# Kernel optimization log

Hardware: AMD Instinct MI355X
Metric: run time of the kernel (lower is better)

Reference implementation:

```python
import jax, jax.numpy as jnp
import numpy as np

N, D, P, R, T, K = 200000, 128, 4096, 4, 3, 16

def setup_inputs() -> dict:
    key = jax.random.key(0)
    ks = jax.random.split(key, 9)
    return {
        "node_embeds": jax.random.normal(ks[0], (N, D), jnp.float32),
        "node_pairs": jax.random.randint(ks[1], (P, 2), 0, N),
        "node_type_ids": jax.random.randint(ks[2], (N,), 0, T),
        "neighbor_idx": jax.random.randint(ks[3], (P, 2, R, K), 0, N),
        "delta_t": jax.random.uniform(ks[4], (P, 2, R, K), jnp.float32),
        "W_phi": jax.random.normal(ks[5], (T, D, D), jnp.float32) * 0.05,
        "W_zeta": jax.random.normal(ks[6], (2 * D,), jnp.float32) * 0.05,
        "W_beta_w": jax.random.normal(ks[7], (R, D, D), jnp.float32) * 0.05,
        "W_beta_b": jax.random.normal(ks[8], (R, D), jnp.float32) * 0.05,
    }

def reference(node_embeds, node_pairs, node_type_ids, neighbor_idx, delta_t,
              W_phi, W_zeta, W_beta_w, W_beta_b):
    n = node_embeds.shape[0]
    # per-node type-specific linear: compute all types then select (T small)
    H_all = jnp.einsum('nd,tde->tne', node_embeds, W_phi)        # [T,N,D]
    H = H_all[node_type_ids, jnp.arange(n)]                      # [N,D]
    # micro attention: e = W_zeta([h_n; h_s]) * exp(-dt), softmax over K neighbors
    zn, zs = W_zeta[:D], W_zeta[D:]
    h_n = H[neighbor_idx]                                        # [P,2,R,K,D]
    e_n = jnp.einsum('psrkd,d->psrk', h_n, zn)
    e_s = jnp.einsum('psd,d->ps', H[node_pairs], zs)             # [P,2]
    e = (e_n + e_s[:, :, None, None]) * jnp.exp(-delta_t)        # [P,2,R,K]
    alpha = jax.nn.softmax(e, axis=-1)
    # meso: attention-weighted aggregation per relation, then per-relation linear
    h_nei = node_embeds[neighbor_idx]                            # [P,2,R,K,D]
    h_agg = jnp.einsum('psrk,psrkd->psrd', alpha, h_nei)         # [P,2,R,D]
    h_beta = jnp.einsum('psrd,rde->psre', h_agg, W_beta_w) + W_beta_b
    # macro: average over both pair sides and relations, sigmoid combine
    x_tilde = h_beta.mean(axis=(1, 2))                           # [P,D]
    return jax.nn.sigmoid(x_tilde)
```

## Files before the change

### kernel.cpp

```cpp
#include <hip/hip_runtime.h>
#include <hip/hip_bf16.h>

#define NN 200000
#define D 128
#define P 4096
#define R 4
#define T 3
#define K 16

__device__ __forceinline__ float bf2f(unsigned int u) {
    union { unsigned int i; float f; } c;
    c.i = u << 16;
    return c.f;
}
__device__ __forceinline__ unsigned short f2bf(float x) {
    union { float f; unsigned int i; } c; c.f = x;
    unsigned int r = c.i + 0x7FFFu + ((c.i >> 16) & 1u);
    return (unsigned short)(r >> 16);
}
__device__ __forceinline__ float ldE(const void* p, size_t i, int f32) {
    return f32 ? ((const float*)p)[i] : bf2f(((const unsigned short*)p)[i]);
}
__device__ __forceinline__ void ld8(const void* p, size_t off, int f32, float* o) {
    if (f32) {
        const float* q = (const float*)p + off;
        float4 a = *(const float4*)q;
        float4 b = *(const float4*)(q + 4);
        o[0]=a.x; o[1]=a.y; o[2]=a.z; o[3]=a.w;
        o[4]=b.x; o[5]=b.y; o[6]=b.z; o[7]=b.w;
    } else {
        uint4 r = *(const uint4*)((const unsigned short*)p + off);
        o[0]=bf2f(r.x & 0xffffu); o[1]=bf2f(r.x >> 16);
        o[2]=bf2f(r.y & 0xffffu); o[3]=bf2f(r.y >> 16);
        o[4]=bf2f(r.z & 0xffffu); o[5]=bf2f(r.z >> 16);
        o[6]=bf2f(r.w & 0xffffu); o[7]=bf2f(r.w >> 16);
    }
}

__global__ void prep_kernel(const unsigned short* __restrict__ emb_u,
                            const void* __restrict__ W_phi,
                            const void* __restrict__ W_zeta,
                            int* __restrict__ gflag,
                            float* __restrict__ ws_v, float* __restrict__ ws_u) {
    __shared__ int sbad[2];
    const int tid = threadIdx.x;
    const int t   = blockIdx.x;
    int bad = 0;
    #pragma unroll
    for (int i = 0; i < 4; ++i) {
        unsigned short u = emb_u[(size_t)(blockIdx.x * 512 + tid * 4 + i) * 2 * 97];
        unsigned int e = (u >> 7) & 0xFFu;
        if (e >= 147u) bad = 1;
    }
    int anyb = __any(bad) ? 1 : 0;
    if ((tid & 63) == 0) sbad[tid >> 6] = anyb;
    __syncthreads();
    const int f32 = sbad[0] | sbad[1];
    if (t == 0 && tid == 0) *gflag = f32;

    const int d = tid;
    const size_t rb = (size_t)(t * D + d) * D;
    float av = 0.f, au = 0.f;
    for (int e = 0; e < D; e += 8) {
        float w[8], zn[8], zs[8];
        ld8(W_phi, rb + e, f32, w);
        ld8(W_zeta, e, f32, zn);
        ld8(W_zeta, D + e, f32, zs);
        #pragma unroll
        for (int q = 0; q < 8; ++q) { av += w[q] * zn[q]; au += w[q] * zs[q]; }
    }
    ws_v[t * D + d] = av;
    ws_u[t * D + d] = au;
}

__global__ __launch_bounds__(256, 4) void fused_all(
    const void* __restrict__ emb,
    const int* __restrict__ pairs,
    const int* __restrict__ types,
    const int* __restrict__ nbr,
    const void* __restrict__ dlt,
    const void* __restrict__ W_bw,
    const void* __restrict__ W_bb,
    const float* __restrict__ ws_v,
    const float* __restrict__ ws_u,
    const int* __restrict__ flag,
    void* __restrict__ out)
{
    __shared__ __align__(16) float vsh[T * D];
    __shared__ __align__(16) float ush[T * D];
    __shared__ __align__(16) float gsh[2][2][R][D];
    __shared__ __align__(16) float ysh[2][2][D];

    const int f32  = *flag;
    const int tid  = threadIdx.x;
    const int wv   = tid >> 6;
    const int l    = tid & 63;
    const int pr   = wv >> 1;
    const int s    = wv & 1;
    const int p    = blockIdx.x * 2 + pr;
    const int rsub = l >> 4;
    const int ch   = l & 15;
    const int base = p * 2 * R * K + s * 64;

    for (int i = tid; i < T * D; i += 256) { vsh[i] = ws_v[i]; ush[i] = ws_u[i]; }
    __syncthreads();

    const int nb  = nbr[base + l];
    const float dtv = ldE(dlt, (size_t)base + l, f32);
    const int tp  = types[nb];

    float es;
    {
        int ns = pairs[p * 2 + s];
        int ts = types[ns];
        float a = ldE(emb, (size_t)ns * D + 2 * l,     f32) * ush[ts * D + 2 * l]
                + ldE(emb, (size_t)ns * D + 2 * l + 1, f32) * ush[ts * D + 2 * l + 1];
        #pragma unroll
        for (int off = 1; off <= 32; off <<= 1) a += __shfl_xor(a, off, 64);
        es = a;
    }

    const unsigned short* eu = (const unsigned short*)emb;

    if (!f32) {
        int snb[4];
        uint4 cur[4], nxt[4];
        #pragma unroll
        for (int i = 0; i < 4; ++i) snb[i] = __shfl(nb, i * 4 + rsub, 64);
        #pragma unroll
        for (int i = 0; i < 4; ++i)
            cur[i] = *(const uint4*)(eu + (size_t)snb[i] * D + ch * 8);

        #pragma unroll
        for (int r = 0; r < R; ++r) {
            float sdt[4]; int stp[4];
            #pragma unroll
            for (int i = 0; i < 4; ++i) {
                int srcl = r * 16 + i * 4 + rsub;
                sdt[i] = __shfl(dtv, srcl, 64);
                stp[i] = __shfl(tp,  srcl, 64);
            }
            if (r < 3) {
                #pragma unroll
                for (int i = 0; i < 4; ++i) snb[i] = __shfl(nb, (r + 1) * 16 + i * 4 + rsub, 64);
                #pragma unroll
                for (int i = 0; i < 4; ++i)
                    nxt[i] = *(const uint4*)(eu + (size_t)snb[i] * D + ch * 8);
            }
            float ef[4];
            #pragma unroll
            for (int i = 0; i < 4; ++i) {
                const float* vp = vsh + stp[i] * D + ch * 8;
                float4 v0 = *(const float4*)vp;
                float4 v1 = *(const float4*)(vp + 4);
                float a = 0.f;
                a += bf2f(cur[i].x & 0xffffu) * v0.x + bf2f(cur[i].x >> 16) * v0.y;
                a += bf2f(cur[i].y & 0xffffu) * v0.z + bf2f(cur[i].y >> 16) * v0.w;
                a += bf2f(cur[i].z & 0xffffu) * v1.x + bf2f(cur[i].z >> 16) * v1.y;
                a += bf2f(cur[i].w & 0xffffu) * v1.z + bf2f(cur[i].w >> 16) * v1.w;
                #pragma unroll
                for (int off = 1; off <= 8; off <<= 1) a += __shfl_xor(a, off, 64);
                ef[i] = (a + es) * __expf(-sdt[i]);
            }
            float m = fmaxf(fmaxf(ef[0], ef[1]), fmaxf(ef[2], ef[3]));
            m = fmaxf(m, __shfl_xor(m, 16, 64));
            m = fmaxf(m, __shfl_xor(m, 32, 64));
            float al[4], ssum = 0.f;
            #pragma unroll
            for (int i = 0; i < 4; ++i) { al[i] = __expf(ef[i] - m); ssum += al[i]; }
            ssum += __shfl_xor(ssum, 16, 64);
            ssum += __shfl_xor(ssum, 32, 64);
            float inv = 1.f / ssum;
            float acc[8] = {0.f,0.f,0.f,0.f,0.f,0.f,0.f,0.f};
            #pragma unroll
            for (int i = 0; i < 4; ++i) {
                float a = al[i] * inv;
                acc[0] += a * bf2f(cur[i].x & 0xffffu); acc[1] += a * bf2f(cur[i].x >> 16);
                acc[2] += a * bf2f(cur[i].y & 0xffffu); acc[3] += a * bf2f(cur[i].y >> 16);
                acc[4] += a * bf2f(cur[i].z & 0xffffu); acc[5] += a * bf2f(cur[i].z >> 16);
                acc[6] += a * bf2f(cur[i].w & 0xffffu); acc[7] += a * bf2f(cur[i].w >> 16);
            }
            #pragma unroll
            for (int q = 0; q < 8; ++q) {
                acc[q] += __shfl_xor(acc[q], 16, 64);
                acc[q] += __shfl_xor(acc[q], 32, 64);
            }
            if (rsub == 0) {
                *(float4*)(&gsh[pr][s][r][ch * 8])     = make_float4(acc[0], acc[1], acc[2], acc[3]);
                *(float4*)(&gsh[pr][s][r][ch * 8 + 4]) = make_float4(acc[4], acc[5], acc[6], acc[7]);
            }
            #pragma unroll
            for (int i = 0; i < 4; ++i) cur[i] = nxt[i];
        }
    } else {
        #pragma unroll
        for (int r = 0; r < R; ++r) {
            int snb[4]; float sdt[4]; int stp[4];
            #pragma unroll
            for (int i = 0; i < 4; ++i) {
                int srcl = r * 16 + i * 4 + rsub;
                snb[i] = __shfl(nb,  srcl, 64);
                sdt[i] = __shfl(dtv, srcl, 64);
                stp[i] = __shfl(tp,  srcl, 64);
            }
            float rv[4][8];
            #pragma unroll
            for (int i = 0; i < 4; ++i) ld8(emb, (size_t)snb[i] * D + ch * 8, 1, rv[i]);
            float ef[4];
            #pragma unroll
            for (int i = 0; i < 4; ++i) {
                const float* vp = vsh + stp[i] * D + ch * 8;
                float a = 0.f;
                #pragma unroll
                for (int q = 0; q < 8; ++q) a += rv[i][q] * vp[q];
                #pragma unroll
                for (int off = 1; off <= 8; off <<= 1) a += __shfl_xor(a, off, 64);
                ef[i] = (a + es) * __expf(-sdt[i]);
            }
            float m = fmaxf(fmaxf(ef[0], ef[1]), fmaxf(ef[2], ef[3]));
            m = fmaxf(m, __shfl_xor(m, 16, 64));
            m = fmaxf(m, __shfl_xor(m, 32, 64));
            float al[4], ssum = 0.f;
            #pragma unroll
            for (int i = 0; i < 4; ++i) { al[i] = __expf(ef[i] - m); ssum += al[i]; }
            ssum += __shfl_xor(ssum, 16, 64);
            ssum += __shfl_xor(ssum, 32, 64);
            float inv = 1.f / ssum;
            float acc[8] = {0.f,0.f,0.f,0.f,0.f,0.f,0.f,0.f};
            #pragma unroll
            for (int i = 0; i < 4; ++i) {
                float a = al[i] * inv;
                #pragma unroll
                for (int q = 0; q < 8; ++q) acc[q] += a * rv[i][q];
            }
            #pragma unroll
            for (int q = 0; q < 8; ++q) {
                acc[q] += __shfl_xor(acc[q], 16, 64);
                acc[q] += __shfl_xor(acc[q], 32, 64);
            }
            if (rsub == 0) {
                *(float4*)(&gsh[pr][s][r][ch * 8])     = make_float4(acc[0], acc[1], acc[2], acc[3]);
                *(float4*)(&gsh[pr][s][r][ch * 8 + 4]) = make_float4(acc[4], acc[5], acc[6], acc[7]);
            }
        }
    }
    __syncthreads();

    float y[8] = {0.f,0.f,0.f,0.f,0.f,0.f,0.f,0.f};
    const unsigned short* Wu = (const unsigned short*)W_bw;
    #pragma unroll
    for (int rr = 0; rr < 2; ++rr) {
        const int r = s * 2 + rr;
        #pragma unroll 8
        for (int dd = 0; dd < 32; ++dd) {
            const int d = rsub * 32 + dd;
            float gd = gsh[pr][0][r][d] + gsh[pr][1][r][d];
            size_t wo = ((size_t)(r * D + d)) * D + ch * 8;
            if (!f32) {
                uint4 wr = *(const uint4*)(Wu + wo);
                y[0] += gd * bf2f(wr.x & 0xffffu); y[1] += gd * bf2f(wr.x >> 16);
                y[2] += gd * bf2f(wr.y & 0xffffu); y[3] += gd * bf2f(wr.y >> 16);
                y[4] += gd * bf2f(wr.z & 0xffffu); y[5] += gd * bf2f(wr.z >> 16);
                y[6] += gd * bf2f(wr.w & 0xffffu); y[7] += gd * bf2f(wr.w >> 16);
            } else {
                float wb[8]; ld8(W_bw, wo, 1, wb);
                #pragma unroll
                for (int q = 0; q < 8; ++q) y[q] += gd * wb[q];
            }
        }
    }
    #pragma unroll
    for (int q = 0; q < 8; ++q) {
        y[q] += __shfl_xor(y[q], 16, 64);
        y[q] += __shfl_xor(y[q], 32, 64);
    }
    if (rsub == 0) {
        *(float4*)(&ysh[pr][s][ch * 8])     = make_float4(y[0], y[1], y[2], y[3]);
        *(float4*)(&ysh[pr][s][ch * 8 + 4]) = make_float4(y[4], y[5], y[6], y[7]);
    }
    __syncthreads();

    if (s == 0 && rsub == 0) {
        float bs[8] = {0.f,0.f,0.f,0.f,0.f,0.f,0.f,0.f};
        #pragma unroll
        for (int r = 0; r < R; ++r) {
            float bb[8]; ld8(W_bb, (size_t)r * D + ch * 8, f32, bb);
            #pragma unroll
            for (int q = 0; q < 8; ++q) bs[q] += bb[q];
        }
        float o[8];
        #pragma unroll
        for (int q = 0; q < 8; ++q) {
            int e = ch * 8 + q;
            float x = (ysh[pr][0][e] + ysh[pr][1][e] + 2.f * bs[q]) * 0.125f;
            o[q] = 1.f / (1.f + __expf(-x));
        }
        size_t ob = (size_t)p * D + ch * 8;
        if (f32) {
            *(float4*)((float*)out + ob)     = make_float4(o[0], o[1], o[2], o[3]);
            *(float4*)((float*)out + ob + 4) = make_float4(o[4], o[5], o[6], o[7]);
        } else {
            uint4 pk;
            pk.x = (unsigned int)f2bf(o[0]) | ((unsigned int)f2bf(o[1]) << 16);
            pk.y = (unsigned int)f2bf(o[2]) | ((unsigned int)f2bf(o[3]) << 16);
            pk.z = (unsigned int)f2bf(o[4]) | ((unsigned int)f2bf(o[5]) << 16);
            pk.w = (unsigned int)f2bf(o[6]) | ((unsigned int)f2bf(o[7]) << 16);
            *(uint4*)((unsigned short*)out + ob) = pk;
        }
    }
}

extern "C" void kernel_launch(void* const* d_in, const int* in_sizes, int n_in,
                              void* d_out, int out_size, void* d_ws, size_t ws_size,
                              hipStream_t stream) {
    const void* emb    = d_in[0];
    const int*  pairs  = (const int*)d_in[1];
    const int*  types  = (const int*)d_in[2];
    const int*  nbr    = (const int*)d_in[3];
    const void* dlt    = d_in[4];
    const void* W_phi  = d_in[5];
    const void* W_zeta = d_in[6];
    const void* W_bw   = d_in[7];
    const void* W_bb   = d_in[8];

    int*   flag = (int*)d_ws;
    float* ws_v = (float*)d_ws + 64;
    float* ws_u = ws_v + T * D;

    prep_kernel<<<dim3(T), dim3(128), 0, stream>>>((const unsigned short*)emb,
                                                   W_phi, W_zeta, flag, ws_v, ws_u);
    fused_all<<<dim3(P / 2), dim3(256), 0, stream>>>(emb, pairs, types, nbr, dlt,
                                                     W_bw, W_bb, ws_v, ws_u, flag, d_out);
}
```

Before: 244.9 us.

## Assign one wave per (side, relation) with one pair per 512-thread block

Restructures the fused kernel so each 512-thread block handles one pair and each of its 8 waves processes one (side, relation) slice, replacing the per-wave serial loop over four relations. All neighbor gathers are issued up front, before the shared-memory staging barrier, so memory latency overlaps the setup. The W_beta projection is redistributed across all waves with a staggered row order and a reduction through shared memory. The change raises memory parallelism and occupancy, at the cost of more blocks, extra barriers and more weight re-reads per pair.

```diff
diff --git a/kernel.cpp b/kernel.cpp
--- a/kernel.cpp
+++ b/kernel.cpp
@@ -73,7 +73,7 @@
     ws_u[t * D + d] = au;
 }
 
-__global__ __launch_bounds__(256, 4) void fused_all(
+__global__ __launch_bounds__(512, 8) void fused_all(
     const void* __restrict__ emb,
     const int* __restrict__ pairs,
     const int* __restrict__ types,
@@ -88,31 +88,49 @@
 {
     __shared__ __align__(16) float vsh[T * D];
     __shared__ __align__(16) float ush[T * D];
-    __shared__ __align__(16) float gsh[2][2][R][D];
-    __shared__ __align__(16) float ysh[2][2][D];
+    __shared__ __align__(16) float gsh[2][R][D];
+    __shared__ __align__(16) float gsum[R][D];
+    __shared__ __align__(16) float ysh[R][D];
 
     const int f32  = *flag;
     const int tid  = threadIdx.x;
     const int wv   = tid >> 6;
     const int l    = tid & 63;
-    const int pr   = wv >> 1;
-    const int s    = wv & 1;
-    const int p    = blockIdx.x * 2 + pr;
+    const int s    = wv >> 2;
+    const int r    = wv & 3;
+    const int p    = blockIdx.x;
     const int rsub = l >> 4;
     const int ch   = l & 15;
-    const int base = p * 2 * R * K + s * 64;
-
-    for (int i = tid; i < T * D; i += 256) { vsh[i] = ws_v[i]; ush[i] = ws_u[i]; }
-    __syncthreads();
-
-    const int nb  = nbr[base + l];
-    const float dtv = ldE(dlt, (size_t)base + l, f32);
-    const int tp  = types[nb];
+    const int base = p * 2 * R * K + s * R * K + r * K;
+
+    const int k   = l & 15;
+    const int nb  = nbr[base + k];
+    const float dtv = ldE(dlt, (size_t)(base + k), f32);
+    const int ns  = pairs[p * 2 + s];
+
+    int snb[4];
+    #pragma unroll
+    for (int i = 0; i < 4; ++i) snb[i] = __shfl(nb, i * 4 + rsub, 64);
+
+    const unsigned short* eu = (const unsigned short*)emb;
+    uint4 cur[4];
+    float rv[4][8];
+    if (!f32) {
+        #pragma unroll
+        for (int i = 0; i < 4; ++i)
+            cur[i] = *(const uint4*)(eu + (size_t)snb[i] * D + ch * 8);
+    } else {
+        #pragma unroll
+        for (int i = 0; i < 4; ++i) ld8(emb, (size_t)snb[i] * D + ch * 8, 1, rv[i]);
+    }
+    const int tp = types[nb];
+    const int ts = types[ns];
+
+    for (int i = tid; i < T * D; i += 512) { vsh[i] = ws_v[i]; ush[i] = ws_u[i]; }
+    __syncthreads();
 
     float es;
     {
-        int ns = pairs[p * 2 + s];
-        int ts = types[ns];
         float a = ldE(emb, (size_t)ns * D + 2 * l,     f32) * ush[ts * D + 2 * l]
                 + ldE(emb, (size_t)ns * D + 2 * l + 1, f32) * ush[ts * D + 2 * l + 1];
         #pragma unroll
@@ -120,182 +138,137 @@
         es = a;
     }
 
-    const unsigned short* eu = (const unsigned short*)emb;
-
+    float sdt[4]; int stp[4];
+    #pragma unroll
+    for (int i = 0; i < 4; ++i) {
+        sdt[i] = __shfl(dtv, i * 4 + rsub, 64);
+        stp[i] = __shfl(tp,  i * 4 + rsub, 64);
+    }
+
+    float ef[4];
     if (!f32) {
-        int snb[4];
-        uint4 cur[4], nxt[4];
-        #pragma unroll
-        for (int i = 0; i < 4; ++i) snb[i] = __shfl(nb, i * 4 + rsub, 64);
-        #pragma unroll
-        for (int i = 0; i < 4; ++i)
-            cur[i] = *(const uint4*)(eu + (size_t)snb[i] * D + ch * 8);
-
-        #pragma unroll
-        for (int r = 0; r < R; ++r) {
-            float sdt[4]; int stp[4];
-            #pragma unroll
-            for (int i = 0; i < 4; ++i) {
-                int srcl = r * 16 + i * 4 + rsub;
-                sdt[i] = __shfl(dtv, srcl, 64);
-                stp[i] = __shfl(tp,  srcl, 64);
-            }
-            if (r < 3) {
-                #pragma unroll
-                for (int i = 0; i < 4; ++i) snb[i] = __shfl(nb, (r + 1) * 16 + i * 4 + rsub, 64);
-                #pragma unroll
-                for (int i = 0; i < 4; ++i)
-                    nxt[i] = *(const uint4*)(eu + (size_t)snb[i] * D + ch * 8);
-            }
-            float ef[4];
-            #pragma unroll
-            for (int i = 0; i < 4; ++i) {
-                const float* vp = vsh + stp[i] * D + ch * 8;
-                float4 v0 = *(const float4*)vp;
-                float4 v1 = *(const float4*)(vp + 4);
-                float a = 0.f;
-                a += bf2f(cur[i].x & 0xffffu) * v0.x + bf2f(cur[i].x >> 16) * v0.y;
-                a += bf2f(cur[i].y & 0xffffu) * v0.z + bf2f(cur[i].y >> 16) * v0.w;
-                a += bf2f(cur[i].z & 0xffffu) * v1.x + bf2f(cur[i].z >> 16) * v1.y;
-                a += bf2f(cur[i].w & 0xffffu) * v1.z + bf2f(cur[i].w >> 16) * v1.w;
-                #pragma unroll
-                for (int off = 1; off <= 8; off <<= 1) a += __shfl_xor(a, off, 64);
-                ef[i] = (a + es) * __expf(-sdt[i]);
-            }
-            float m = fmaxf(fmaxf(ef[0], ef[1]), fmaxf(ef[2], ef[3]));
-            m = fmaxf(m, __shfl_xor(m, 16, 64));
-            m = fmaxf(m, __shfl_xor(m, 32, 64));
-            float al[4], ssum = 0.f;
-            #pragma unroll
-            for (int i = 0; i < 4; ++i) { al[i] = __expf(ef[i] - m); ssum += al[i]; }
-            ssum += __shfl_xor(ssum, 16, 64);
-            ssum += __shfl_xor(ssum, 32, 64);
-            float inv = 1.f / ssum;
-            float acc[8] = {0.f,0.f,0.f,0.f,0.f,0.f,0.f,0.f};
-            #pragma unroll
-            for (int i = 0; i < 4; ++i) {
-                float a = al[i] * inv;
-                acc[0] += a * bf2f(cur[i].x & 0xffffu); acc[1] += a * bf2f(cur[i].x >> 16);
-                acc[2] += a * bf2f(cur[i].y & 0xffffu); acc[3] += a * bf2f(cur[i].y >> 16);
-                acc[4] += a * bf2f(cur[i].z & 0xffffu); acc[5] += a * bf2f(cur[i].z >> 16);
-                acc[6] += a * bf2f(cur[i].w & 0xffffu); acc[7] += a * bf2f(cur[i].w >> 16);
-            }
-            #pragma unroll
-            for (int q = 0; q < 8; ++q) {
-                acc[q] += __shfl_xor(acc[q], 16, 64);
-                acc[q] += __shfl_xor(acc[q], 32, 64);
-            }
-            if (rsub == 0) {
-                *(float4*)(&gsh[pr][s][r][ch * 8])     = make_float4(acc[0], acc[1], acc[2], acc[3]);
-                *(float4*)(&gsh[pr][s][r][ch * 8 + 4]) = make_float4(acc[4], acc[5], acc[6], acc[7]);
-            }
-            #pragma unroll
-            for (int i = 0; i < 4; ++i) cur[i] = nxt[i];
+        #pragma unroll
+        for (int i = 0; i < 4; ++i) {
+            const float* vp = vsh + stp[i] * D + ch * 8;
+            float4 v0 = *(const float4*)vp;
+            float4 v1 = *(const float4*)(vp + 4);
+            float a = 0.f;
+            a += bf2f(cur[i].x & 0xffffu) * v0.x + bf2f(cur[i].x >> 16) * v0.y;
+            a += bf2f(cur[i].y & 0xffffu) * v0.z + bf2f(cur[i].y >> 16) * v0.w;
+            a += bf2f(cur[i].z & 0xffffu) * v1.x + bf2f(cur[i].z >> 16) * v1.y;
+            a += bf2f(cur[i].w & 0xffffu) * v1.z + bf2f(cur[i].w >> 16) * v1.w;
+            #pragma unroll
+            for (int off = 1; off <= 8; off <<= 1) a += __shfl_xor(a, off, 64);
+            ef[i] = (a + es) * __expf(-sdt[i]);
         }
     } else {
         #pragma unroll
-        for (int r = 0; r < R; ++r) {
-            int snb[4]; float sdt[4]; int stp[4];
-            #pragma unroll
-            for (int i = 0; i < 4; ++i) {
-                int srcl = r * 16 + i * 4 + rsub;
-                snb[i] = __shfl(nb,  srcl, 64);
-                sdt[i] = __shfl(dtv, srcl, 64);
-                stp[i] = __shfl(tp,  srcl, 64);
-            }
-            float rv[4][8];
-            #pragma unroll
-            for (int i = 0; i < 4; ++i) ld8(emb, (size_t)snb[i] * D + ch * 8, 1, rv[i]);
-            float ef[4];
-            #pragma unroll
-            for (int i = 0; i < 4; ++i) {
-                const float* vp = vsh + stp[i] * D + ch * 8;
-                float a = 0.f;
-                #pragma unroll
-                for (int q = 0; q < 8; ++q) a += rv[i][q] * vp[q];
-                #pragma unroll
-                for (int off = 1; off <= 8; off <<= 1) a += __shfl_xor(a, off, 64);
-                ef[i] = (a + es) * __expf(-sdt[i]);
-            }
-            float m = fmaxf(fmaxf(ef[0], ef[1]), fmaxf(ef[2], ef[3]));
-            m = fmaxf(m, __shfl_xor(m, 16, 64));
-            m = fmaxf(m, __shfl_xor(m, 32, 64));
-            float al[4], ssum = 0.f;
-            #pragma unroll
-            for (int i = 0; i < 4; ++i) { al[i] = __expf(ef[i] - m); ssum += al[i]; }
-            ssum += __shfl_xor(ssum, 16, 64);
-            ssum += __shfl_xor(ssum, 32, 64);
-            float inv = 1.f / ssum;
-            float acc[8] = {0.f,0.f,0.f,0.f,0.f,0.f,0.f,0.f};
-            #pragma unroll
-            for (int i = 0; i < 4; ++i) {
-                float a = al[i] * inv;
-                #pragma unroll
-                for (int q = 0; q < 8; ++q) acc[q] += a * rv[i][q];
-            }
-            #pragma unroll
-            for (int q = 0; q < 8; ++q) {
-                acc[q] += __shfl_xor(acc[q], 16, 64);
-                acc[q] += __shfl_xor(acc[q], 32, 64);
-            }
-            if (rsub == 0) {
-                *(float4*)(&gsh[pr][s][r][ch * 8])     = make_float4(acc[0], acc[1], acc[2], acc[3]);
-                *(float4*)(&gsh[pr][s][r][ch * 8 + 4]) = make_float4(acc[4], acc[5], acc[6], acc[7]);
-            }
-        }
+        for (int i = 0; i < 4; ++i) {
+            const float* vp = vsh + stp[i] * D + ch * 8;
+            float a = 0.f;
+            #pragma unroll
+            for (int q = 0; q < 8; ++q) a += rv[i][q] * vp[q];
+            #pragma unroll
+            for (int off = 1; off <= 8; off <<= 1) a += __shfl_xor(a, off, 64);
+            ef[i] = (a + es) * __expf(-sdt[i]);
+        }
+    }
+
+    float m = fmaxf(fmaxf(ef[0], ef[1]), fmaxf(ef[2], ef[3]));
+    m = fmaxf(m, __shfl_xor(m, 16, 64));
+    m = fmaxf(m, __shfl_xor(m, 32, 64));
+    float al[4], ssum = 0.f;
+    #pragma unroll
+    for (int i = 0; i < 4; ++i) { al[i] = __expf(ef[i] - m); ssum += al[i]; }
+    ssum += __shfl_xor(ssum, 16, 64);
+    ssum += __shfl_xor(ssum, 32, 64);
+    float inv = 1.f / ssum;
+
+    float acc[8] = {0.f,0.f,0.f,0.f,0.f,0.f,0.f,0.f};
+    if (!f32) {
+        #pragma unroll
+        for (int i = 0; i < 4; ++i) {
+            float a = al[i] * inv;
+            acc[0] += a * bf2f(cur[i].x & 0xffffu); acc[1] += a * bf2f(cur[i].x >> 16);
+            acc[2] += a * bf2f(cur[i].y & 0xffffu); acc[3] += a * bf2f(cur[i].y >> 16);
+            acc[4] += a * bf2f(cur[i].z & 0xffffu); acc[5] += a * bf2f(cur[i].z >> 16);
+            acc[6] += a * bf2f(cur[i].w & 0xffffu); acc[7] += a * bf2f(cur[i].w >> 16);
+        }
+    } else {
+        #pragma unroll
+        for (int i = 0; i < 4; ++i) {
+            float a = al[i] * inv;
+            #pragma unroll
+            for (int q = 0; q < 8; ++q) acc[q] += a * rv[i][q];
+        }
+    }
+    #pragma unroll
+    for (int q = 0; q < 8; ++q) {
+        acc[q] += __shfl_xor(acc[q], 16, 64);
+        acc[q] += __shfl_xor(acc[q], 32, 64);
+    }
+    if (rsub == 0) {
+        *(float4*)(&gsh[s][r][ch * 8])     = make_float4(acc[0], acc[1], acc[2], acc[3]);
+        *(float4*)(&gsh[s][r][ch * 8 + 4]) = make_float4(acc[4], acc[5], acc[6], acc[7]);
+    }
+    __syncthreads();
+
+    {
+        const int r2 = tid >> 7, d2 = tid & 127;
+        gsum[r2][d2] = gsh[0][r2][d2] + gsh[1][r2][d2];
     }
     __syncthreads();
 
     float y[8] = {0.f,0.f,0.f,0.f,0.f,0.f,0.f,0.f};
+    const int ch8  = l & 7;
+    const int dgrp = l >> 3;
     const unsigned short* Wu = (const unsigned short*)W_bw;
-    #pragma unroll
-    for (int rr = 0; rr < 2; ++rr) {
-        const int r = s * 2 + rr;
-        #pragma unroll 8
-        for (int dd = 0; dd < 32; ++dd) {
-            const int d = rsub * 32 + dd;
-            float gd = gsh[pr][0][r][d] + gsh[pr][1][r][d];
-            size_t wo = ((size_t)(r * D + d)) * D + ch * 8;
-            if (!f32) {
-                uint4 wr = *(const uint4*)(Wu + wo);
-                y[0] += gd * bf2f(wr.x & 0xffffu); y[1] += gd * bf2f(wr.x >> 16);
-                y[2] += gd * bf2f(wr.y & 0xffffu); y[3] += gd * bf2f(wr.y >> 16);
-                y[4] += gd * bf2f(wr.z & 0xffffu); y[5] += gd * bf2f(wr.z >> 16);
-                y[6] += gd * bf2f(wr.w & 0xffffu); y[7] += gd * bf2f(wr.w >> 16);
-            } else {
-                float wb[8]; ld8(W_bw, wo, 1, wb);
-                #pragma unroll
-                for (int q = 0; q < 8; ++q) y[q] += gd * wb[q];
-            }
+    #pragma unroll 4
+    for (int dd = 0; dd < 16; ++dd) {
+        const int d = dgrp * 16 + ((dd + 2 * dgrp) & 15);
+        const float gd = gsum[r][d];
+        const size_t wo = ((size_t)(r * D + d)) * D + s * 64 + ch8 * 8;
+        if (!f32) {
+            uint4 wr = *(const uint4*)(Wu + wo);
+            y[0] += gd * bf2f(wr.x & 0xffffu); y[1] += gd * bf2f(wr.x >> 16);
+            y[2] += gd * bf2f(wr.y & 0xffffu); y[3] += gd * bf2f(wr.y >> 16);
+            y[4] += gd * bf2f(wr.z & 0xffffu); y[5] += gd * bf2f(wr.z >> 16);
+            y[6] += gd * bf2f(wr.w & 0xffffu); y[7] += gd * bf2f(wr.w >> 16);
+        } else {
+            float wb[8]; ld8(W_bw, wo, 1, wb);
+            #pragma unroll
+            for (int q = 0; q < 8; ++q) y[q] += gd * wb[q];
         }
     }
     #pragma unroll
     for (int q = 0; q < 8; ++q) {
+        y[q] += __shfl_xor(y[q], 8, 64);
         y[q] += __shfl_xor(y[q], 16, 64);
         y[q] += __shfl_xor(y[q], 32, 64);
     }
-    if (rsub == 0) {
-        *(float4*)(&ysh[pr][s][ch * 8])     = make_float4(y[0], y[1], y[2], y[3]);
-        *(float4*)(&ysh[pr][s][ch * 8 + 4]) = make_float4(y[4], y[5], y[6], y[7]);
-    }
-    __syncthreads();
-
-    if (s == 0 && rsub == 0) {
+    if (dgrp == 0) {
+        *(float4*)(&ysh[r][s * 64 + ch8 * 8])     = make_float4(y[0], y[1], y[2], y[3]);
+        *(float4*)(&ysh[r][s * 64 + ch8 * 8 + 4]) = make_float4(y[4], y[5], y[6], y[7]);
+    }
+    __syncthreads();
+
+    if (wv == 0 && l < 16) {
+        const int c = l;
         float bs[8] = {0.f,0.f,0.f,0.f,0.f,0.f,0.f,0.f};
         #pragma unroll
-        for (int r = 0; r < R; ++r) {
-            float bb[8]; ld8(W_bb, (size_t)r * D + ch * 8, f32, bb);
+        for (int rr = 0; rr < R; ++rr) {
+            float bb[8]; ld8(W_bb, (size_t)rr * D + c * 8, f32, bb);
             #pragma unroll
             for (int q = 0; q < 8; ++q) bs[q] += bb[q];
         }
         float o[8];
         #pragma unroll
         for (int q = 0; q < 8; ++q) {
-            int e = ch * 8 + q;
-            float x = (ysh[pr][0][e] + ysh[pr][1][e] + 2.f * bs[q]) * 0.125f;
+            const int e = c * 8 + q;
+            float x = (ysh[0][e] + ysh[1][e] + ysh[2][e] + ysh[3][e] + 2.f * bs[q]) * 0.125f;
             o[q] = 1.f / (1.f + __expf(-x));
         }
-        size_t ob = (size_t)p * D + ch * 8;
+        size_t ob = (size_t)p * D + c * 8;
         if (f32) {
             *(float4*)((float*)out + ob)     = make_float4(o[0], o[1], o[2], o[3]);
             *(float4*)((float*)out + ob + 4) = make_float4(o[4], o[5], o[6], o[7]);
@@ -329,6 +302,6 @@
 
     prep_kernel<<<dim3(T), dim3(128), 0, stream>>>((const unsigned short*)emb,
                                                    W_phi, W_zeta, flag, ws_v, ws_u);
-    fused_all<<<dim3(P / 2), dim3(256), 0, stream>>>(emb, pairs, types, nbr, dlt,
-                                                     W_bw, W_bb, ws_v, ws_u, flag, d_out);
-}
+    fused_all<<<dim3(P), dim3(512), 0, stream>>>(emb, pairs, types, nbr, dlt,
+                                                 W_bw, W_bb, ws_v, ws_u, flag, d_out);
+}
```

Result: slower. 392.7 us (+60.3%).

## Hoist first gathers above shared-memory fill and raise occupancy target

Applied to the files above, without the earlier changes.

Moves the first neighbor-row gathers and the source-node embedding load ahead of the shared-memory table fill and its barrier, so their latency overlaps the barrier. It also raises the launch-bounds occupancy hint from 4 to 8 blocks per CU, which caps registers and may cause spills. The fp32 path now reloads rows instead of keeping them in registers. The W_beta loop order is staggered per rsub group, which appears aimed at reducing shared-memory bank conflicts.

```diff
diff --git a/kernel.cpp b/kernel.cpp
--- a/kernel.cpp
+++ b/kernel.cpp
@@ -73,7 +73,7 @@
     ws_u[t * D + d] = au;
 }
 
-__global__ __launch_bounds__(256, 4) void fused_all(
+__global__ __launch_bounds__(256, 8) void fused_all(
     const void* __restrict__ emb,
     const int* __restrict__ pairs,
     const int* __restrict__ types,
@@ -102,35 +102,43 @@
     const int ch   = l & 15;
     const int base = p * 2 * R * K + s * 64;
 
-    for (int i = tid; i < T * D; i += 256) { vsh[i] = ws_v[i]; ush[i] = ws_u[i]; }
-    __syncthreads();
-
     const int nb  = nbr[base + l];
     const float dtv = ldE(dlt, (size_t)base + l, f32);
     const int tp  = types[nb];
+    const int ns  = pairs[p * 2 + s];
+    const int ts  = types[ns];
+
+    const unsigned short* eu = (const unsigned short*)emb;
+
+    int snb[4];
+    #pragma unroll
+    for (int i = 0; i < 4; ++i) snb[i] = __shfl(nb, i * 4 + rsub, 64);
+    uint4 cur[4] = {};
+    float ee0, ee1;
+    if (!f32) {
+        #pragma unroll
+        for (int i = 0; i < 4; ++i)
+            cur[i] = *(const uint4*)(eu + (size_t)snb[i] * D + ch * 8);
+        unsigned int w2 = *(const unsigned int*)(eu + (size_t)ns * D + 2 * l);
+        ee0 = bf2f(w2 & 0xffffu); ee1 = bf2f(w2 >> 16);
+    } else {
+        float2 f2 = *(const float2*)((const float*)emb + (size_t)ns * D + 2 * l);
+        ee0 = f2.x; ee1 = f2.y;
+    }
+
+    for (int i = tid; i < T * D; i += 256) { vsh[i] = ws_v[i]; ush[i] = ws_u[i]; }
+    __syncthreads();
 
     float es;
     {
-        int ns = pairs[p * 2 + s];
-        int ts = types[ns];
-        float a = ldE(emb, (size_t)ns * D + 2 * l,     f32) * ush[ts * D + 2 * l]
-                + ldE(emb, (size_t)ns * D + 2 * l + 1, f32) * ush[ts * D + 2 * l + 1];
+        float a = ee0 * ush[ts * D + 2 * l] + ee1 * ush[ts * D + 2 * l + 1];
         #pragma unroll
         for (int off = 1; off <= 32; off <<= 1) a += __shfl_xor(a, off, 64);
         es = a;
     }
 
-    const unsigned short* eu = (const unsigned short*)emb;
-
     if (!f32) {
-        int snb[4];
-        uint4 cur[4], nxt[4];
-        #pragma unroll
-        for (int i = 0; i < 4; ++i) snb[i] = __shfl(nb, i * 4 + rsub, 64);
-        #pragma unroll
-        for (int i = 0; i < 4; ++i)
-            cur[i] = *(const uint4*)(eu + (size_t)snb[i] * D + ch * 8);
-
+        uint4 nxt[4];
         #pragma unroll
         for (int r = 0; r < R; ++r) {
             float sdt[4]; int stp[4];
@@ -141,11 +149,12 @@
                 stp[i] = __shfl(tp,  srcl, 64);
             }
             if (r < 3) {
-                #pragma unroll
-                for (int i = 0; i < 4; ++i) snb[i] = __shfl(nb, (r + 1) * 16 + i * 4 + rsub, 64);
+                int snb2[4];
+                #pragma unroll
+                for (int i = 0; i < 4; ++i) snb2[i] = __shfl(nb, (r + 1) * 16 + i * 4 + rsub, 64);
                 #pragma unroll
                 for (int i = 0; i < 4; ++i)
-                    nxt[i] = *(const uint4*)(eu + (size_t)snb[i] * D + ch * 8);
+                    nxt[i] = *(const uint4*)(eu + (size_t)snb2[i] * D + ch * 8);
             }
             float ef[4];
             #pragma unroll
@@ -195,24 +204,23 @@
     } else {
         #pragma unroll
         for (int r = 0; r < R; ++r) {
-            int snb[4]; float sdt[4]; int stp[4];
+            int snbL[4]; float sdt[4]; int stp[4];
             #pragma unroll
             for (int i = 0; i < 4; ++i) {
                 int srcl = r * 16 + i * 4 + rsub;
-                snb[i] = __shfl(nb,  srcl, 64);
+                snbL[i] = __shfl(nb,  srcl, 64);
                 sdt[i] = __shfl(dtv, srcl, 64);
                 stp[i] = __shfl(tp,  srcl, 64);
             }
-            float rv[4][8];
-            #pragma unroll
-            for (int i = 0; i < 4; ++i) ld8(emb, (size_t)snb[i] * D + ch * 8, 1, rv[i]);
             float ef[4];
             #pragma unroll
             for (int i = 0; i < 4; ++i) {
                 const float* vp = vsh + stp[i] * D + ch * 8;
+                float rv[8];
+                ld8(emb, (size_t)snbL[i] * D + ch * 8, 1, rv);
                 float a = 0.f;
                 #pragma unroll
-                for (int q = 0; q < 8; ++q) a += rv[i][q] * vp[q];
+                for (int q = 0; q < 8; ++q) a += rv[q] * vp[q];
                 #pragma unroll
                 for (int off = 1; off <= 8; off <<= 1) a += __shfl_xor(a, off, 64);
                 ef[i] = (a + es) * __expf(-sdt[i]);
@@ -230,8 +238,10 @@
             #pragma unroll
             for (int i = 0; i < 4; ++i) {
                 float a = al[i] * inv;
-                #pragma unroll
-                for (int q = 0; q < 8; ++q) acc[q] += a * rv[i][q];
+                float rv[8];
+                ld8(emb, (size_t)snbL[i] * D + ch * 8, 1, rv);
+                #pragma unroll
+                for (int q = 0; q < 8; ++q) acc[q] += a * rv[q];
             }
             #pragma unroll
             for (int q = 0; q < 8; ++q) {
@@ -253,7 +263,7 @@
         const int r = s * 2 + rr;
         #pragma unroll 8
         for (int dd = 0; dd < 32; ++dd) {
-            const int d = rsub * 32 + dd;
+            const int d = rsub * 32 + ((dd + 8 * rsub) & 31);
             float gd = gsh[pr][0][r][d] + gsh[pr][1][r][d];
             size_t wo = ((size_t)(r * D + d)) * D + ch * 8;
             if (!f32) {
```

New measurement: 292.5 us. +19.4%, slower.
